# Kernel optimization log

Hardware: AMD Instinct MI355X
Metric: run time of the kernel (lower is better)

The kernel has to match this reference:

```python
import jax, jax.numpy as jnp
import numpy as np

SIG_EPS = 0.1
IN_DIM = 256
OUT_DIM = 64


def setup_inputs() -> dict:
    key = jax.random.key(0)
    ks = jax.random.split(key, 6)
    B, S, Q = 32, 512, 512
    return {
        "phi_support": jax.random.normal(ks[0], (B, S, IN_DIM), jnp.float32),
        "y_support": jax.random.normal(ks[1], (B, S, OUT_DIM), jnp.float32),
        "phi_query": jax.random.normal(ks[2], (B, Q, IN_DIM), jnp.float32),
        "y_query": jax.random.normal(ks[3], (B, Q, OUT_DIM), jnp.float32),
        # learned parameters (K init'd to zeros in torch, use small randn for a non-trivial test)
        "K": jax.random.normal(ks[4], (IN_DIM, OUT_DIM), jnp.float32) * 0.02,
        "L_asym": jax.random.normal(ks[5], (IN_DIM, IN_DIM), jnp.float32) * 0.1,
    }


def reference(phi_support, y_support, phi_query, y_query, K, L_asym):
    sig_eps = jnp.float32(SIG_EPS)
    log_sig_eps = jnp.log(sig_eps)
    out_dim = K.shape[1]

    L = L_asym @ L_asym.T  # [I, I]
    # nobs > 0 branch (n_support = 512)
    posterior_L = jnp.einsum('bsi,bsj->bij', phi_support, phi_support) + L[None]  # [B,I,I]
    posterior_L_inv = jnp.linalg.inv(posterior_L)
    rhs = jnp.einsum('bsi,bso->bio', phi_support, y_support) + (L @ K)[None]  # [B,I,O]
    posterior_K = posterior_L_inv @ rhs  # [B,I,O]

    mu_pred = phi_query @ posterior_K  # [B,Q,O]
    # spread_fac = 1 + diag quadratic form phi Linv phi^T  -> [B,Q]
    spread_fac = 1.0 + jnp.einsum('bqi,bij,bqj->bq', phi_query, posterior_L_inv, phi_query)
    eye_eps = jnp.eye(out_dim, dtype=phi_query.dtype) * sig_eps
    sig_pred = spread_fac[..., None, None] * eye_eps  # [B,Q,O,O]

    # predictive_nll: inverse of sig_pred is an exactly scaled identity, so the
    # quadratic form y^T inv(sig_pred) y == ||y||^2 / (spread_fac * sig_eps) (same math)
    diff = y_query - mu_pred
    quadf = jnp.sum(diff * diff, axis=-1) / (spread_fac * sig_eps)  # [B,Q]
    logdet = out_dim * (jnp.log(spread_fac) + log_sig_eps)  # [B,Q]
    predictive_nll = logdet.mean() + quadf.mean()

    return (mu_pred, sig_pred, predictive_nll)
```

## Files before the change

### kernel.cpp

```cpp
#include <hip/hip_runtime.h>
#include <math.h>

#define B 32
#define S 512
#define Q 512
#define I 256
#define O 64
#define SIG_EPS 0.1f
#define LOG_SIG_EPS (-2.3025850929940457f)

#define WS_L 0
#define WS_T1 65536
#define WS_LKT 81920
#define WS_M0 98304
#define WS_M1 2195456
#define WS_RHST 4292608
#define WS_D 4816896
#define WS_SPF 5079040
#define WS_U16 5095488
#define U_PTH 0
#define U_PTL 4194304
#define U_YTH 8388608
#define U_YTL 9437184
#define U_IVH 10485760
#define U_IVL 12582912

#define OUT_MU_ELEMS (B * Q * O)
#define OUT_SIG_ELEMS (B * Q * O * O)
#define OUT_NLL_IDX (OUT_MU_ELEMS + OUT_SIG_ELEMS)

typedef short short8 __attribute__((ext_vector_type(8)));
typedef float f32x4 __attribute__((ext_vector_type(4)));
#define MFMA16(a, b, c) __builtin_amdgcn_mfma_f32_16x16x32_bf16(a, b, c, 0, 0, 0)

struct Params {
  const float *phi_s, *y_s, *phi_q, *y_q, *Km, *La;
  float *Lm, *T1, *LKT, *M0, *M1, *RHST, *Dbuf, *spws;
  unsigned short *PTh, *PTl, *YTh, *YTl, *IVh, *IVl;
  float *mu, *nll;
  float4 *sig;
};

__device__ __forceinline__ f32x4 mfma3(short8 ah, short8 al, short8 bh, short8 bl, f32x4 c) {
  c = MFMA16(ah, bh, c);
  c = MFMA16(ah, bl, c);
  c = MFMA16(al, bh, c);
  return c;
}

__device__ __forceinline__ unsigned short f2bf(float x) {
  unsigned int u = __float_as_uint(x);
  return (unsigned short)((u + 0x7fffu + ((u >> 16) & 1u)) >> 16);
}
__device__ __forceinline__ float bf2f(unsigned short h) { return __uint_as_float(((unsigned int)h) << 16); }
__device__ __forceinline__ void split2(float x, unsigned short& h, unsigned short& l) {
  h = f2bf(x);
  l = f2bf(x - bf2f(h));
}
__device__ __forceinline__ void split4(float4 v, uint2& H, uint2& L) {
  unsigned short h0, h1, h2, h3, l0, l1, l2, l3;
  split2(v.x, h0, l0); split2(v.y, h1, l1); split2(v.z, h2, l2); split2(v.w, h3, l3);
  H.x = (unsigned)h0 | ((unsigned)h1 << 16); H.y = (unsigned)h2 | ((unsigned)h3 << 16);
  L.x = (unsigned)l0 | ((unsigned)l1 << 16); L.y = (unsigned)l2 | ((unsigned)l3 << 16);
}
__device__ __forceinline__ void cvt8(const float* p, short8& h8, short8& l8) {
  float4 a = *(const float4*)p;
  float4 b = *(const float4*)(p + 4);
  uint2 H0, L0, H1, L1;
  split4(a, H0, L0); split4(b, H1, L1);
  union { uint2 q[2]; short8 s; } uh, ul;
  uh.q[0] = H0; uh.q[1] = H1; ul.q[0] = L0; ul.q[1] = L1;
  h8 = uh.s; l8 = ul.s;
}
__device__ __forceinline__ short8 ld8(const unsigned short* p) { return *(const short8*)(const void*)p; }

__device__ __forceinline__ void fma4x4(const float4 av, const float4 bv, float acc[4][4]) {
  const float ar[4] = {av.x, av.y, av.z, av.w};
  const float br[4] = {bv.x, bv.y, bv.z, bv.w};
#pragma unroll
  for (int i = 0; i < 4; ++i)
#pragma unroll
    for (int j = 0; j < 4; ++j) acc[i][j] += ar[i] * br[j];
}

__device__ __forceinline__ void load_direct64(float* dst, int ds, const float* src, int ss, int t) {
#pragma unroll
  for (int m = 0; m < 4; ++m) {
    int r = (t >> 4) + 16 * m, c4 = (t & 15) * 4;
    *(float4*)&dst[r * ds + c4] = *(const float4*)&src[(size_t)r * ss + c4];
  }
}
__device__ __forceinline__ void load_trans64(float* dst, int ds, const float* src, int ss, int t) {
#pragma unroll
  for (int m = 0; m < 4; ++m) {
    int r = (t >> 4) + 16 * m, c4 = (t & 15) * 4;
    float4 v = *(const float4*)&src[(size_t)r * ss + c4];
    dst[(c4 + 0) * ds + r] = v.x;
    dst[(c4 + 1) * ds + r] = v.y;
    dst[(c4 + 2) * ds + r] = v.z;
    dst[(c4 + 3) * ds + r] = v.w;
  }
}
template <int SA, int SB>
__device__ __forceinline__ void gemm64(const float* At, const float* Bs, int tr, int tc, float acc[4][4]) {
#pragma unroll 8
  for (int kk = 0; kk < 64; ++kk) {
    float4 a = *(const float4*)&At[kk * SA + tr * 4];
    float4 b = *(const float4*)&Bs[kk * SB + tc * 4];
    fma4x4(a, b, acc);
  }
}

#define SC4(V) V.x *= pivinv; V.y *= pivinv; V.z *= pivinv; V.w *= pivinv
#define UP4(V, R) V.x -= g * R.x; V.y -= g * R.y; V.z -= g * R.z; V.w -= g * R.w

template <int TS>
__device__ void gj64(const float* T, float* rowbuf, float* Dout, int t) {
  int r = t >> 2, q = t & 3;
  int lane = t & 63;
  float4 A0 = *(const float4*)&T[r * TS + q * 16 + 0];
  float4 A1 = *(const float4*)&T[r * TS + q * 16 + 4];
  float4 A2 = *(const float4*)&T[r * TS + q * 16 + 8];
  float4 A3 = *(const float4*)&T[r * TS + q * 16 + 12];
#define IC(c) (((q * 16 + (c)) == r) ? 1.f : 0.f)
  float4 I0 = make_float4(IC(0), IC(1), IC(2), IC(3));
  float4 I1 = make_float4(IC(4), IC(5), IC(6), IC(7));
  float4 I2 = make_float4(IC(8), IC(9), IC(10), IC(11));
  float4 I3 = make_float4(IC(12), IC(13), IC(14), IC(15));
#undef IC
  for (int p = 0; p < 64; ++p) {
    float* RA = rowbuf + (p & 1) * 128;
    float* RI = RA + 64;
    if (r == p) {
      ((float4*)&RA[q * 16])[0] = A0; ((float4*)&RA[q * 16])[1] = A1;
      ((float4*)&RA[q * 16])[2] = A2; ((float4*)&RA[q * 16])[3] = A3;
      ((float4*)&RI[q * 16])[0] = I0; ((float4*)&RI[q * 16])[1] = I1;
      ((float4*)&RI[q * 16])[2] = I2; ((float4*)&RI[q * 16])[3] = I3;
    }
    __syncthreads();
    float pivinv = 1.0f / RA[p];
    int sidx = p & 15;
    float4 blk = (sidx < 8) ? ((sidx < 4) ? A0 : A1) : ((sidx < 12) ? A2 : A3);
    int sc = sidx & 3;
    float ap = (sc == 0) ? blk.x : (sc == 1) ? blk.y : (sc == 2) ? blk.z : blk.w;
    float f = __shfl(ap, (lane & ~3) | (p >> 4), 64);
    float4 ra0 = ((const float4*)&RA[q * 16])[0], ra1 = ((const float4*)&RA[q * 16])[1];
    float4 ra2 = ((const float4*)&RA[q * 16])[2], ra3 = ((const float4*)&RA[q * 16])[3];
    float4 ri0 = ((const float4*)&RI[q * 16])[0], ri1 = ((const float4*)&RI[q * 16])[1];
    float4 ri2 = ((const float4*)&RI[q * 16])[2], ri3 = ((const float4*)&RI[q * 16])[3];
    if (r == p) {
      SC4(A0); SC4(A1); SC4(A2); SC4(A3);
      SC4(I0); SC4(I1); SC4(I2); SC4(I3);
    } else {
      float g = f * pivinv;
      UP4(A0, ra0); UP4(A1, ra1); UP4(A2, ra2); UP4(A3, ra3);
      UP4(I0, ri0); UP4(I1, ri1); UP4(I2, ri2); UP4(I3, ri3);
    }
  }
  ((float4*)&Dout[r * 64 + q * 16])[0] = I0;
  ((float4*)&Dout[r * 64 + q * 16])[1] = I1;
  ((float4*)&Dout[r * 64 + q * 16])[2] = I2;
  ((float4*)&Dout[r * 64 + q * 16])[3] = I3;
}

__global__ __launch_bounds__(256) void k_front(Params p) {
  __shared__ float smem[4352];
  int w = blockIdx.x, t = threadIdx.x;
  if (w == 0 && t == 0) p.nll[0] = 0.f;
  if (w < 1280) {
    unsigned short* Hs = (unsigned short*)smem;
    unsigned short* Lo = Hs + 64 * 68;
    const float* src;
    unsigned short *dh, *dl;
    int sstride;
    if (w < 1024) {
      int b = w >> 5, r = w & 31, ic = r >> 3, sc = r & 7;
      src = p.phi_s + ((size_t)b * 512 + sc * 64) * 256 + ic * 64;
      sstride = 256;
      size_t d0 = ((size_t)b * 256 + ic * 64) * 512 + sc * 64;
      dh = p.PTh + d0; dl = p.PTl + d0;
    } else {
      int qq = w - 1024, b = qq >> 3, sc = qq & 7;
      src = p.y_s + ((size_t)b * 512 + sc * 64) * 64;
      sstride = 64;
      size_t d0 = ((size_t)b * 64) * 512 + sc * 64;
      dh = p.YTh + d0; dl = p.YTl + d0;
    }
    int c = t & 63, rb = (t >> 6) * 16;
#pragma unroll
    for (int m = 0; m < 16; ++m) {
      int s = rb + m;
      float x = src[(size_t)s * sstride + c];
      unsigned short h, l;
      split2(x, h, l);
      Hs[c * 68 + s] = h;
      Lo[c * 68 + s] = l;
    }
    __syncthreads();
    int il0 = t >> 4, c4 = (t & 15) * 4;
#pragma unroll
    for (int m = 0; m < 4; ++m) {
      int il = il0 + 16 * m;
      uint2 H, L;
      H.x = (unsigned)Hs[il * 68 + c4] | ((unsigned)Hs[il * 68 + c4 + 1] << 16);
      H.y = (unsigned)Hs[il * 68 + c4 + 2] | ((unsigned)Hs[il * 68 + c4 + 3] << 16);
      L.x = (unsigned)Lo[il * 68 + c4] | ((unsigned)Lo[il * 68 + c4 + 1] << 16);
      L.y = (unsigned)Lo[il * 68 + c4 + 2] | ((unsigned)Lo[il * 68 + c4 + 3] << 16);
      *(uint2*)&dh[(size_t)il * 512 + c4] = H;
      *(uint2*)&dl[(size_t)il * 512 + c4] = L;
    }
  } else {
    int blk2 = w - 1280;
    float* sA = smem;
    float* sB = smem + 1088;
    int tr = t >> 4, tc = t & 15;
    float acc[4][4] = {};
    if (blk2 < 16) {
      int i0 = (blk2 >> 2) * 64, j0 = (blk2 & 3) * 64;
      for (int ks = 0; ks < 256; ks += 16) {
        __syncthreads();
#pragma unroll
        for (int m = 0; m < 4; ++m) {
          int r = (t >> 4) + 16 * m, kk = t & 15;
          sA[kk * 68 + r] = p.La[(size_t)(i0 + r) * 256 + ks + kk];
          sB[kk * 68 + r] = p.La[(size_t)(j0 + r) * 256 + ks + kk];
        }
        __syncthreads();
#pragma unroll
        for (int kk = 0; kk < 16; ++kk) {
          float4 a = *(const float4*)&sA[kk * 68 + tr * 4];
          float4 bv = *(const float4*)&sB[kk * 68 + tc * 4];
          fma4x4(a, bv, acc);
        }
      }
#pragma unroll
      for (int mi = 0; mi < 4; ++mi) {
        float4 v = {acc[mi][0], acc[mi][1], acc[mi][2], acc[mi][3]};
        *(float4*)&p.Lm[(size_t)(i0 + tr * 4 + mi) * 256 + j0 + tc * 4] = v;
      }
    } else {
      int i0 = (blk2 - 16) * 64;
      for (int ks = 0; ks < 256; ks += 16) {
        __syncthreads();
#pragma unroll
        for (int m = 0; m < 4; ++m) {
          int kk = (t >> 6) + 4 * m, c = t & 63;
          sA[kk * 68 + c] = p.La[(size_t)(ks + kk) * 256 + i0 + c];
          sB[kk * 68 + c] = p.Km[(size_t)(ks + kk) * 64 + c];
        }
        __syncthreads();
#pragma unroll
        for (int kk = 0; kk < 16; ++kk) {
          float4 a = *(const float4*)&sA[kk * 68 + tr * 4];
          float4 bv = *(const float4*)&sB[kk * 68 + tc * 4];
          fma4x4(a, bv, acc);
        }
      }
#pragma unroll
      for (int mi = 0; mi < 4; ++mi) {
        float4 v = {acc[mi][0], acc[mi][1], acc[mi][2], acc[mi][3]};
        *(float4*)&p.T1[(size_t)(i0 + tr * 4 + mi) * 64 + tc * 4] = v;
      }
    }
  }
}

__global__ __launch_bounds__(256) void k_gram(Params p) {
  __shared__ float smem[5632];
  float* trbuf = smem;
  float* Ws = smem + 4352;
  float* rowb = smem + 5376;
  int b = blockIdx.x, u = blockIdx.y, t = threadIdx.x;
  if (u == 14) {
    if (b >= 4) return;
    int i0 = b * 64;
    int tr = t >> 4, tc = t & 15;
    float acc[4][4] = {};
    for (int ks = 0; ks < 256; ks += 16) {
      __syncthreads();
#pragma unroll
      for (int m = 0; m < 4; ++m) {
        trbuf[(t & 15) * 68 + (t >> 4) + 16 * m] = p.La[(size_t)(i0 + (t >> 4) + 16 * m) * 256 + ks + (t & 15)];
        Ws[((t >> 6) + 4 * m) * 64 + (t & 63)] = p.T1[(size_t)(ks + (t >> 6) + 4 * m) * 64 + (t & 63)];
      }
      __syncthreads();
#pragma unroll
      for (int kk = 0; kk < 16; ++kk) {
        float4 a = *(const float4*)&trbuf[kk * 68 + tr * 4];
        float4 bv = *(const float4*)&Ws[kk * 64 + tc * 4];
        fma4x4(a, bv, acc);
      }
    }
    __syncthreads();
#pragma unroll
    for (int mi = 0; mi < 4; ++mi)
#pragma unroll
      for (int cj = 0; cj < 4; ++cj) trbuf[(tr * 4 + mi) * 68 + tc * 4 + cj] = acc[mi][cj];
    __syncthreads();
    int rr0 = t >> 4, cc4 = (t & 15) * 4;
#pragma unroll
    for (int m = 0; m < 4; ++m) {
      int rr = rr0 + 16 * m;
      float4 v = {trbuf[(cc4 + 0) * 68 + rr], trbuf[(cc4 + 1) * 68 + rr], trbuf[(cc4 + 2) * 68 + rr],
                  trbuf[(cc4 + 3) * 68 + rr]};
      *(float4*)&p.LKT[(size_t)rr * 256 + i0 + cc4] = v;
    }
    return;
  }
  const int TIa[14] = {0, 0, 0, 0, 1, 1, 1, 2, 2, 3, 0, 1, 2, 3};
  const int TJa[14] = {0, 1, 2, 3, 1, 2, 3, 2, 3, 3, 0, 0, 0, 0};
  bool isR = (u >= 10);
  int it = TIa[u], jt = TJa[u];
  int i0 = it * 64, j0 = isR ? 0 : jt * 64;
  int lane = t & 63, w = t >> 6, wr = w >> 1, wc = w & 1;
  const unsigned short* Ah = p.PTh + (size_t)b * 256 * 512;
  const unsigned short* Al = p.PTl + (size_t)b * 256 * 512;
  const unsigned short* Bh = isR ? (p.YTh + (size_t)b * 64 * 512) : Ah;
  const unsigned short* Bl = isR ? (p.YTl + (size_t)b * 64 * 512) : Al;
  int ra0 = i0 + wr * 32 + (lane & 15);
  int rb0 = j0 + wc * 32 + (lane & 15);
  int klane = (lane >> 4) * 8;
  f32x4 acc[2][2] = {};
  for (int ks = 0; ks < 512; ks += 32) {
    int kk = ks + klane;
    short8 a0h = ld8(Ah + (size_t)ra0 * 512 + kk);
    short8 a1h = ld8(Ah + (size_t)(ra0 + 16) * 512 + kk);
    short8 a0l = ld8(Al + (size_t)ra0 * 512 + kk);
    short8 a1l = ld8(Al + (size_t)(ra0 + 16) * 512 + kk);
    short8 b0h = ld8(Bh + (size_t)rb0 * 512 + kk);
    short8 b1h = ld8(Bh + (size_t)(rb0 + 16) * 512 + kk);
    short8 b0l = ld8(Bl + (size_t)rb0 * 512 + kk);
    short8 b1l = ld8(Bl + (size_t)(rb0 + 16) * 512 + kk);
    acc[0][0] = mfma3(a0h, a0l, b0h, b0l, acc[0][0]);
    acc[0][1] = mfma3(a0h, a0l, b1h, b1l, acc[0][1]);
    acc[1][0] = mfma3(a1h, a1l, b0h, b0l, acc[1][0]);
    acc[1][1] = mfma3(a1h, a1l, b1h, b1l, acc[1][1]);
  }
#pragma unroll
  for (int ti = 0; ti < 2; ++ti)
#pragma unroll
    for (int tj = 0; tj < 2; ++tj)
#pragma unroll
      for (int r = 0; r < 4; ++r)
        trbuf[(wr * 32 + ti * 16 + (lane >> 4) * 4 + r) * 68 + wc * 32 + tj * 16 + (lane & 15)] = acc[ti][tj][r];
  __syncthreads();
  int rr0 = t >> 4, cc4 = (t & 15) * 4;
  if (!isR) {
    float* Mb = p.M0 + (size_t)b * 65536;
    bool d00 = (it == 0 && jt == 0);
#pragma unroll
    for (int m = 0; m < 4; ++m) {
      int rr = rr0 + 16 * m;
      float4 v = *(float4*)&trbuf[rr * 68 + cc4];
      float4 lv = *(const float4*)&p.Lm[(size_t)(i0 + rr) * 256 + j0 + cc4];
      v.x += lv.x; v.y += lv.y; v.z += lv.z; v.w += lv.w;
      *(float4*)&Mb[(size_t)(i0 + rr) * 256 + j0 + cc4] = v;
      if (d00) *(float4*)&trbuf[rr * 68 + cc4] = v;
    }
    if (it != jt) {
#pragma unroll
      for (int m = 0; m < 4; ++m) {
        int rr = rr0 + 16 * m;
        float4 v = {trbuf[(cc4 + 0) * 68 + rr], trbuf[(cc4 + 1) * 68 + rr], trbuf[(cc4 + 2) * 68 + rr],
                    trbuf[(cc4 + 3) * 68 + rr]};
        float4 lv = *(const float4*)&p.Lm[(size_t)(j0 + rr) * 256 + i0 + cc4];
        v.x += lv.x; v.y += lv.y; v.z += lv.z; v.w += lv.w;
        *(float4*)&Mb[(size_t)(j0 + rr) * 256 + i0 + cc4] = v;
      }
    }
    if (d00) {
      __syncthreads();
      gj64<68>(trbuf, rowb, p.Dbuf + (size_t)b * 4096, t);
    }
  } else {
#pragma unroll
    for (int m = 0; m < 4; ++m) {
      int rr = rr0 + 16 * m;
      float4 v = {trbuf[(cc4 + 0) * 68 + rr], trbuf[(cc4 + 1) * 68 + rr], trbuf[(cc4 + 2) * 68 + rr],
                  trbuf[(cc4 + 3) * 68 + rr]};
      *(float4*)&p.RHST[((size_t)b * 64 + rr) * 256 + i0 + cc4] = v;
    }
  }
}

__global__ __launch_bounds__(256) void k_st(Params p, int kb) {
  __shared__ float smem[13056];
  float* shA = smem;
  float* shB = smem + 4352;
  float* shD = smem + 8448;
  float* rowb = smem + 12800;
  int b = blockIdx.x, u = blockIdx.y, t = threadIdx.x;
  if (u == 16) {
    float4* R4 = (float4*)(p.RHST + (size_t)b * 16384);
    const float4* L4 = (const float4*)p.LKT;
#pragma unroll
    for (int m = 0; m < 16; ++m) {
      int idx = m * 256 + t;
      float4 a = R4[idx];
      float4 l = L4[idx];
      a.x += l.x; a.y += l.y; a.z += l.z; a.w += l.w;
      R4[idx] = a;
    }
    return;
  }
  int i = u >> 2, j = u & 3;
  int tr = t >> 4, tc = t & 15;
  const float* Ms = ((kb & 1) ? p.M1 : p.M0) + (size_t)b * 65536;
  float* Md = ((kb & 1) ? p.M0 : p.M1) + (size_t)b * 65536;
  const float* Din = p.Dbuf + (size_t)(kb & 1) * (B * 4096) + (size_t)b * 4096;
  float* Dout = p.Dbuf + (size_t)((kb + 1) & 1) * (B * 4096) + (size_t)b * 4096;
  bool last = (kb == 3);
  unsigned short* Yh = p.IVh + (size_t)b * 65536;
  unsigned short* Yl = p.IVl + (size_t)b * 65536;
  auto STORE = [&](int row, int col, float4 v) {
    if (last) {
      uint2 H, L;
      split4(v, H, L);
      *(uint2*)&Yh[(size_t)row * 256 + col] = H;
      *(uint2*)&Yl[(size_t)row * 256 + col] = L;
    } else {
      *(float4*)&Md[(size_t)row * 256 + col] = v;
    }
  };
  bool ik = (i == kb), jk = (j == kb);
  if (ik && jk) {
#pragma unroll
    for (int m = 0; m < 4; ++m) {
      int r = (t >> 4) + 16 * m, c4 = (t & 15) * 4;
      STORE(kb * 64 + r, kb * 64 + c4, *(const float4*)&Din[r * 64 + c4]);
    }
  } else if (ik) {
    float acc[4][4] = {};
    load_trans64(shA, 68, Din, 64, t);
    load_direct64(shB, 64, &Ms[(size_t)(kb * 64) * 256 + j * 64], 256, t);
    __syncthreads();
    gemm64<68, 64>(shA, shB, tr, tc, acc);
    __syncthreads();
#pragma unroll
    for (int mi = 0; mi < 4; ++mi) {
      float4 v = {acc[mi][0], acc[mi][1], acc[mi][2], acc[mi][3]};
      STORE(kb * 64 + tr * 4 + mi, j * 64 + tc * 4, v);
    }
  } else if (jk) {
    float acc[4][4] = {};
    load_trans64(shA, 68, &Ms[(size_t)(i * 64) * 256 + kb * 64], 256, t);
    load_direct64(shB, 64, Din, 64, t);
    __syncthreads();
    gemm64<68, 64>(shA, shB, tr, tc, acc);
    __syncthreads();
#pragma unroll
    for (int mi = 0; mi < 4; ++mi) {
      float4 v = {-acc[mi][0], -acc[mi][1], -acc[mi][2], -acc[mi][3]};
      STORE(i * 64 + tr * 4 + mi, kb * 64 + tc * 4, v);
    }
  } else {
    float acc[4][4] = {};
    load_trans64(shA, 68, Din, 64, t);
    load_direct64(shB, 64, &Ms[(size_t)(kb * 64) * 256 + j * 64], 256, t);
    load_trans64(shD, 68, &Ms[(size_t)(i * 64) * 256 + kb * 64], 256, t);
    __syncthreads();
    gemm64<68, 64>(shA, shB, tr, tc, acc);
    __syncthreads();
#pragma unroll
    for (int mi = 0; mi < 4; ++mi) {
      float4 v = {acc[mi][0], acc[mi][1], acc[mi][2], acc[mi][3]};
      *(float4*)&shB[(tr * 4 + mi) * 64 + tc * 4] = v;
    }
    __syncthreads();
    float acc2[4][4] = {};
    gemm64<68, 64>(shD, shB, tr, tc, acc2);
    bool la = (kb < 3) && (i == kb + 1) && (j == kb + 1);
    if (la) __syncthreads();
#pragma unroll
    for (int mi = 0; mi < 4; ++mi) {
      size_t off = (size_t)(i * 64 + tr * 4 + mi) * 256 + j * 64 + tc * 4;
      float4 old = *(const float4*)&Ms[off];
      float4 v = {old.x - acc2[mi][0], old.y - acc2[mi][1], old.z - acc2[mi][2], old.w - acc2[mi][3]};
      STORE(i * 64 + tr * 4 + mi, j * 64 + tc * 4, v);
      if (la) *(float4*)&shB[(tr * 4 + mi) * 64 + tc * 4] = v;
    }
    if (la) {
      __syncthreads();
      gj64<64>(shB, rowb, Dout, t);
    }
  }
}

__global__ __launch_bounds__(256) void k_tail(Params p) {
  __shared__ float Xlds[32 * 260];
  __shared__ float Gs[64 * 68];
  __shared__ float spf[32];
  __shared__ float ssdl[32];
  int b = blockIdx.x, qb = blockIdx.y * 32, t = threadIdx.x;
  int lane = t & 63, w = t >> 6;
  int klane = (lane >> 4) * 8;
  const float* Pq = p.phi_q + (size_t)b * 512 * 256;

  short8 ah[2][8], al[2][8];
#pragma unroll
  for (int st = 0; st < 2; ++st) {
    int qlane = qb + st * 16 + (lane & 15);
#pragma unroll
    for (int k8 = 0; k8 < 8; ++k8) cvt8(&Pq[(size_t)qlane * 256 + k8 * 32 + klane], ah[st][k8], al[st][k8]);
  }

  const unsigned short* Vh = p.IVh + (size_t)b * 65536;
  const unsigned short* Vl = p.IVl + (size_t)b * 65536;
  for (int jt = w * 4; jt < w * 4 + 4; ++jt) {
    int jrow = jt * 16 + (lane & 15);
    f32x4 acc0 = {}, acc1 = {};
#pragma unroll
    for (int k8 = 0; k8 < 8; ++k8) {
      short8 bh = ld8(Vh + (size_t)jrow * 256 + k8 * 32 + klane);
      short8 bl = ld8(Vl + (size_t)jrow * 256 + k8 * 32 + klane);
      acc0 = mfma3(ah[0][k8], al[0][k8], bh, bl, acc0);
      acc1 = mfma3(ah[1][k8], al[1][k8], bh, bl, acc1);
    }
    int xi = jt * 16 + (lane & 15);
#pragma unroll
    for (int r = 0; r < 4; ++r) {
      Xlds[((lane >> 4) * 4 + r) * 260 + xi] = acc0[r];
      Xlds[(16 + (lane >> 4) * 4 + r) * 260 + xi] = acc1[r];
    }
  }
  __syncthreads();

  {
    int q = t >> 3, c = t & 7;
    const float* Pqr = Pq + (size_t)(qb + q) * 256;
    float sp = 0.f;
#pragma unroll
    for (int i = c * 32; i < c * 32 + 32; i += 4) {
      float4 xv = *(const float4*)&Xlds[q * 260 + i];
      float4 pv = *(const float4*)&Pqr[i];
      sp += xv.x * pv.x + xv.y * pv.y + xv.z * pv.z + xv.w * pv.w;
    }
    sp += __shfl_xor(sp, 1);
    sp += __shfl_xor(sp, 2);
    sp += __shfl_xor(sp, 4);
    if (c == 0) spf[q] = 1.f + sp;
  }

  {
    int q = t >> 3, c = t & 7;
    const float* Gr = p.RHST + (size_t)b * 16384;
    float accv[8] = {};
    for (int ip = 0; ip < 4; ++ip) {
      __syncthreads();
      int grr = t >> 2, gc = (t & 3) * 16;
#pragma unroll
      for (int m = 0; m < 4; ++m)
        *(float4*)&Gs[grr * 68 + gc + m * 4] = *(const float4*)&Gr[(size_t)grr * 256 + ip * 64 + gc + m * 4];
      __syncthreads();
#pragma unroll 2
      for (int i = 0; i < 64; i += 4) {
        float4 xv = *(const float4*)&Xlds[q * 260 + ip * 64 + i];
#pragma unroll
        for (int oo = 0; oo < 8; ++oo) {
          float4 gv = *(const float4*)&Gs[(c + oo * 8) * 68 + i];
          accv[oo] += xv.x * gv.x + xv.y * gv.y + xv.z * gv.z + xv.w * gv.w;
        }
      }
    }
    size_t qg = (size_t)b * 512 + qb + q;
    float ssd8 = 0.f;
#pragma unroll
    for (int oo = 0; oo < 8; ++oo) {
      int o = c + oo * 8;
      p.mu[qg * 64 + o] = accv[oo];
      float d = p.y_q[qg * 64 + o] - accv[oo];
      ssd8 += d * d;
    }
    ssd8 += __shfl_xor(ssd8, 1);
    ssd8 += __shfl_xor(ssd8, 2);
    ssd8 += __shfl_xor(ssd8, 4);
    if (c == 0) ssdl[q] = ssd8;
  }
  __syncthreads();

  if (w == 0) {
    float val = 0.f;
    if (t < 32) {
      float sp = spf[t];
      val = (64.f * (logf(sp) + LOG_SIG_EPS) + ssdl[t] / (sp * SIG_EPS)) * (1.0f / 16384.0f);
    }
#pragma unroll
    for (int off = 32; off; off >>= 1) val += __shfl_down(val, off);
    if (t == 0) atomicAdd(p.nll, val);
  }
  if (t < 32) p.spws[(size_t)b * 512 + qb + t] = spf[t];
}

__global__ __launch_bounds__(256) void k_sig(const float* __restrict__ spws, float4* __restrict__ sig) {
  size_t idx = (size_t)blockIdx.x * 256 + threadIdx.x;
  int p4 = (int)(idx & 15);
  int o = (int)((idx >> 4) & 63);
  size_t bq = idx >> 10;
  float sv = spws[bq] * SIG_EPS;
  float4 v;
  v.x = (p4 * 4 + 0 == o) ? sv : 0.f;
  v.y = (p4 * 4 + 1 == o) ? sv : 0.f;
  v.z = (p4 * 4 + 2 == o) ? sv : 0.f;
  v.w = (p4 * 4 + 3 == o) ? sv : 0.f;
  sig[idx] = v;
}

extern "C" void kernel_launch(void* const* d_in, const int* in_sizes, int n_in, void* d_out, int out_size,
                              void* d_ws, size_t ws_size, hipStream_t stream) {
  float* ws = (float*)d_ws;
  unsigned short* u16b = (unsigned short*)(ws + WS_U16);
  float* out_mu = (float*)d_out;

  Params p;
  p.phi_s = (const float*)d_in[0];
  p.y_s = (const float*)d_in[1];
  p.phi_q = (const float*)d_in[2];
  p.y_q = (const float*)d_in[3];
  p.Km = (const float*)d_in[4];
  p.La = (const float*)d_in[5];
  p.Lm = ws + WS_L;
  p.T1 = ws + WS_T1;
  p.LKT = ws + WS_LKT;
  p.M0 = ws + WS_M0;
  p.M1 = ws + WS_M1;
  p.RHST = ws + WS_RHST;
  p.Dbuf = ws + WS_D;
  p.spws = ws + WS_SPF;
  p.PTh = u16b + U_PTH;
  p.PTl = u16b + U_PTL;
  p.YTh = u16b + U_YTH;
  p.YTl = u16b + U_YTL;
  p.IVh = u16b + U_IVH;
  p.IVl = u16b + U_IVL;
  p.mu = out_mu;
  p.sig = (float4*)(out_mu + OUT_MU_ELEMS);
  p.nll = out_mu + OUT_NLL_IDX;

  k_front<<<1300, 256, 0, stream>>>(p);
  k_gram<<<dim3(B, 15), 256, 0, stream>>>(p);
  k_st<<<dim3(B, 17), 256, 0, stream>>>(p, 0);
  k_st<<<dim3(B, 16), 256, 0, stream>>>(p, 1);
  k_st<<<dim3(B, 16), 256, 0, stream>>>(p, 2);
  k_st<<<dim3(B, 16), 256, 0, stream>>>(p, 3);
  k_tail<<<dim3(B, 16), 256, 0, stream>>>(p);
  k_sig<<<65536, 256, 0, stream>>>(p.spws, p.sig);
}
```

Baseline: 309.4 us.

## Fuse block Gauss-Jordan pivot steps pairwise and write sig output inside tail kernel

The four per-pivot-block Gauss-Jordan sweeps over the 4x4 block matrix become two launches. Each launch eliminates two pivot blocks at once, redundantly recomputing the second pivot's Schur complement and its 64x64 inverse in every block. Separately, the dense sig_pred diagonal fill moves from its own kernel into k_tail, which removes the spread-factor round trip through workspace. Fewer launches and fewer full passes over the 256x256 matrices are traded for extra per-block GEMMs and a replicated 64x64 inversion in each workgroup, and k_tail now has to write the 268 MB sig output itself.

```diff
diff --git a/kernel.cpp b/kernel.cpp
--- a/kernel.cpp
+++ b/kernel.cpp
@@ -16,7 +16,6 @@
 #define WS_M1 2195456
 #define WS_RHST 4292608
 #define WS_D 4816896
-#define WS_SPF 5079040
 #define WS_U16 5095488
 #define U_PTH 0
 #define U_PTL 4194304
@@ -35,7 +34,7 @@
 
 struct Params {
   const float *phi_s, *y_s, *phi_q, *y_q, *Km, *La;
-  float *Lm, *T1, *LKT, *M0, *M1, *RHST, *Dbuf, *spws;
+  float *Lm, *T1, *LKT, *M0, *M1, *RHST, *Dbuf;
   unsigned short *PTh, *PTl, *YTh, *YTl, *IVh, *IVl;
   float *mu, *nll;
   float4 *sig;
@@ -111,11 +110,52 @@
   }
 }
 
+__device__ __forceinline__ void wr_rm(float* dst, const float a[4][4], int tr, int tc) {
+#pragma unroll
+  for (int mi = 0; mi < 4; ++mi) {
+    float4 v = {a[mi][0], a[mi][1], a[mi][2], a[mi][3]};
+    *(float4*)&dst[(tr * 4 + mi) * 68 + tc * 4] = v;
+  }
+}
+__device__ __forceinline__ void wr_tr(float* dst, const float a[4][4], int tr, int tc) {
+#pragma unroll
+  for (int mi = 0; mi < 4; ++mi)
+#pragma unroll
+    for (int cj = 0; cj < 4; ++cj) dst[(tc * 4 + cj) * 68 + tr * 4 + mi] = a[mi][cj];
+}
+__device__ __forceinline__ void sub_from_g(const float* src, int ss, float a[4][4], int tr, int tc) {
+#pragma unroll
+  for (int mi = 0; mi < 4; ++mi) {
+    float4 g = *(const float4*)&src[(size_t)(tr * 4 + mi) * ss + tc * 4];
+    a[mi][0] = g.x - a[mi][0]; a[mi][1] = g.y - a[mi][1];
+    a[mi][2] = g.z - a[mi][2]; a[mi][3] = g.w - a[mi][3];
+  }
+}
+__device__ __forceinline__ void ld_g(const float* src, int ss, float a[4][4], int tr, int tc) {
+#pragma unroll
+  for (int mi = 0; mi < 4; ++mi) {
+    float4 g = *(const float4*)&src[(size_t)(tr * 4 + mi) * ss + tc * 4];
+    a[mi][0] = g.x; a[mi][1] = g.y; a[mi][2] = g.z; a[mi][3] = g.w;
+  }
+}
+__device__ __forceinline__ void negt(float a[4][4]) {
+#pragma unroll
+  for (int mi = 0; mi < 4; ++mi)
+#pragma unroll
+    for (int cj = 0; cj < 4; ++cj) a[mi][cj] = -a[mi][cj];
+}
+__device__ __forceinline__ void cpt(float d[4][4], const float s[4][4]) {
+#pragma unroll
+  for (int mi = 0; mi < 4; ++mi)
+#pragma unroll
+    for (int cj = 0; cj < 4; ++cj) d[mi][cj] = s[mi][cj];
+}
+
 #define SC4(V) V.x *= pivinv; V.y *= pivinv; V.z *= pivinv; V.w *= pivinv
 #define UP4(V, R) V.x -= g * R.x; V.y -= g * R.y; V.z -= g * R.z; V.w -= g * R.w
 
-template <int TS>
-__device__ void gj64(const float* T, float* rowbuf, float* Dout, int t) {
+template <int TS, int OUT>
+__device__ void gj64c(const float* T, float* rowbuf, float* Dout, int t) {
   int r = t >> 2, q = t & 3;
   int lane = t & 63;
   float4 A0 = *(const float4*)&T[r * TS + q * 16 + 0];
@@ -157,11 +197,20 @@
       UP4(I0, ri0); UP4(I1, ri1); UP4(I2, ri2); UP4(I3, ri3);
     }
   }
-  ((float4*)&Dout[r * 64 + q * 16])[0] = I0;
-  ((float4*)&Dout[r * 64 + q * 16])[1] = I1;
-  ((float4*)&Dout[r * 64 + q * 16])[2] = I2;
-  ((float4*)&Dout[r * 64 + q * 16])[3] = I3;
-}
+  if (OUT == 0) {
+    ((float4*)&Dout[r * 64 + q * 16])[0] = I0;
+    ((float4*)&Dout[r * 64 + q * 16])[1] = I1;
+    ((float4*)&Dout[r * 64 + q * 16])[2] = I2;
+    ((float4*)&Dout[r * 64 + q * 16])[3] = I3;
+  } else {
+    ((float4*)&Dout[r * 68 + q * 16])[0] = I0;
+    ((float4*)&Dout[r * 68 + q * 16])[1] = I1;
+    ((float4*)&Dout[r * 68 + q * 16])[2] = I2;
+    ((float4*)&Dout[r * 68 + q * 16])[3] = I3;
+  }
+}
+template <int TS>
+__device__ void gj64(const float* T, float* rowbuf, float* Dout, int t) { gj64c<TS, 0>(T, rowbuf, Dout, t); }
 
 __global__ __launch_bounds__(256) void k_front(Params p) {
   __shared__ float smem[4352];
@@ -383,12 +432,11 @@
   }
 }
 
-__global__ __launch_bounds__(256) void k_st(Params p, int kb) {
-  __shared__ float smem[13056];
-  float* shA = smem;
-  float* shB = smem + 4352;
-  float* shD = smem + 8448;
-  float* rowb = smem + 12800;
+__global__ __launch_bounds__(256) void k_st2(Params p, int a) {
+  __shared__ float shA[64 * 68];
+  __shared__ float shB[64 * 68];
+  __shared__ float shD[64 * 68];
+  __shared__ float rowb[256];
   int b = blockIdx.x, u = blockIdx.y, t = threadIdx.x;
   if (u == 16) {
     float4* R4 = (float4*)(p.RHST + (size_t)b * 16384);
@@ -396,20 +444,21 @@
 #pragma unroll
     for (int m = 0; m < 16; ++m) {
       int idx = m * 256 + t;
-      float4 a = R4[idx];
-      float4 l = L4[idx];
-      a.x += l.x; a.y += l.y; a.z += l.z; a.w += l.w;
-      R4[idx] = a;
+      float4 av = R4[idx];
+      float4 lv = L4[idx];
+      av.x += lv.x; av.y += lv.y; av.z += lv.z; av.w += lv.w;
+      R4[idx] = av;
     }
     return;
   }
+  int tr = t >> 4, tc = t & 15;
   int i = u >> 2, j = u & 3;
-  int tr = t >> 4, tc = t & 15;
-  const float* Ms = ((kb & 1) ? p.M1 : p.M0) + (size_t)b * 65536;
-  float* Md = ((kb & 1) ? p.M0 : p.M1) + (size_t)b * 65536;
-  const float* Din = p.Dbuf + (size_t)(kb & 1) * (B * 4096) + (size_t)b * 4096;
-  float* Dout = p.Dbuf + (size_t)((kb + 1) & 1) * (B * 4096) + (size_t)b * 4096;
-  bool last = (kb == 3);
+  int b2 = a + 1;
+  const float* Ms = (a == 0 ? p.M0 : p.M1) + (size_t)b * 65536;
+  float* Md = p.M1 + (size_t)b * 65536;
+  const float* Din = p.Dbuf + (a == 0 ? 0 : (size_t)B * 4096) + (size_t)b * 4096;
+  float* DoutG = p.Dbuf + (size_t)B * 4096 + (size_t)b * 4096;
+  bool last = (a == 2);
   unsigned short* Yh = p.IVh + (size_t)b * 65536;
   unsigned short* Yl = p.IVl + (size_t)b * 65536;
   auto STORE = [&](int row, int col, float4 v) {
@@ -422,68 +471,126 @@
       *(float4*)&Md[(size_t)row * 256 + col] = v;
     }
   };
-  bool ik = (i == kb), jk = (j == kb);
-  if (ik && jk) {
-#pragma unroll
-    for (int m = 0; m < 4; ++m) {
-      int r = (t >> 4) + 16 * m, c4 = (t & 15) * 4;
-      STORE(kb * 64 + r, kb * 64 + c4, *(const float4*)&Din[r * 64 + c4]);
-    }
-  } else if (ik) {
-    float acc[4][4] = {};
-    load_trans64(shA, 68, Din, 64, t);
-    load_direct64(shB, 64, &Ms[(size_t)(kb * 64) * 256 + j * 64], 256, t);
-    __syncthreads();
-    gemm64<68, 64>(shA, shB, tr, tc, acc);
-    __syncthreads();
+  auto SACC = [&](const float acc[4][4], int r0, int c0) {
 #pragma unroll
     for (int mi = 0; mi < 4; ++mi) {
       float4 v = {acc[mi][0], acc[mi][1], acc[mi][2], acc[mi][3]};
-      STORE(kb * 64 + tr * 4 + mi, j * 64 + tc * 4, v);
-    }
-  } else if (jk) {
-    float acc[4][4] = {};
-    load_trans64(shA, 68, &Ms[(size_t)(i * 64) * 256 + kb * 64], 256, t);
-    load_direct64(shB, 64, Din, 64, t);
-    __syncthreads();
-    gemm64<68, 64>(shA, shB, tr, tc, acc);
-    __syncthreads();
+      STORE(r0 + tr * 4 + mi, c0 + tc * 4, v);
+    }
+  };
+#define TP(r, c) (&Ms[(size_t)((r) * 64) * 256 + (c) * 64])
+
+  bool isDiag = (i == b2 && j == b2);
+  bool isRow = (i == b2 && j != b2);
+  bool isCol = (j == b2 && i != b2);
+  bool gen = (i != b2 && j != b2);
+  bool needTj = (j != b2 && j != a);
+  bool needDrm = (j == a);
+
+  load_trans64(shA, 68, Din, 64, t);
+  load_direct64(shB, 68, TP(a, b2), 256, t);
+  __syncthreads();
+  float t1c[4][4] = {};
+  gemm64<68, 68>(shA, shB, tr, tc, t1c);
+  float tj[4][4] = {};
+  if (needTj) {
+    __syncthreads();
+    load_direct64(shB, 68, TP(a, j), 256, t);
+    __syncthreads();
+    gemm64<68, 68>(shA, shB, tr, tc, tj);
+    __syncthreads();
+    wr_rm(shB, tj, tr, tc);
+  } else if (needDrm) {
+    __syncthreads();
+    load_direct64(shB, 68, Din, 64, t);
+  }
+  __syncthreads();
+  load_trans64(shD, 68, TP(b2, a), 256, t);
+  wr_rm(shA, t1c, tr, tc);
+  __syncthreads();
+  float sbb[4][4] = {};
+  gemm64<68, 68>(shD, shA, tr, tc, sbb);
+  sub_from_g(TP(b2, b2), 256, sbb, tr, tc);
+  float nbj[4][4] = {};
+  if (gen || isRow) {
+    gemm64<68, 68>(shD, shB, tr, tc, nbj);
+    if (j == a) negt(nbj);
+    else sub_from_g(TP(b2, j), 256, nbj, tr, tc);
+  }
+  float nib[4][4] = {}, nij[4][4] = {};
+  if (gen || isCol) {
+    if (i == a) {
+      cpt(nib, t1c);
+      if (gen) {
+        if (j == a) ld_g(Din, 64, nij, tr, tc);
+        else cpt(nij, tj);
+      }
+    } else {
+      __syncthreads();
+      load_trans64(shD, 68, TP(i, a), 256, t);
+      __syncthreads();
+      gemm64<68, 68>(shD, shA, tr, tc, nib);
+      sub_from_g(TP(i, b2), 256, nib, tr, tc);
+      if (gen) {
+        gemm64<68, 68>(shD, shB, tr, tc, nij);
+        if (j == a) negt(nij);
+        else sub_from_g(TP(i, j), 256, nij, tr, tc);
+      }
+    }
+  }
+  __syncthreads();
+  wr_rm(shA, sbb, tr, tc);
+  __syncthreads();
+  gj64c<68, 1>(shA, rowb, shD, t);
+  __syncthreads();
+  if (isDiag) {
 #pragma unroll
     for (int mi = 0; mi < 4; ++mi) {
-      float4 v = {-acc[mi][0], -acc[mi][1], -acc[mi][2], -acc[mi][3]};
-      STORE(i * 64 + tr * 4 + mi, kb * 64 + tc * 4, v);
-    }
-  } else {
-    float acc[4][4] = {};
-    load_trans64(shA, 68, Din, 64, t);
-    load_direct64(shB, 64, &Ms[(size_t)(kb * 64) * 256 + j * 64], 256, t);
-    load_trans64(shD, 68, &Ms[(size_t)(i * 64) * 256 + kb * 64], 256, t);
-    __syncthreads();
-    gemm64<68, 64>(shA, shB, tr, tc, acc);
-    __syncthreads();
-#pragma unroll
-    for (int mi = 0; mi < 4; ++mi) {
-      float4 v = {acc[mi][0], acc[mi][1], acc[mi][2], acc[mi][3]};
-      *(float4*)&shB[(tr * 4 + mi) * 64 + tc * 4] = v;
-    }
-    __syncthreads();
-    float acc2[4][4] = {};
-    gemm64<68, 64>(shD, shB, tr, tc, acc2);
-    bool la = (kb < 3) && (i == kb + 1) && (j == kb + 1);
-    if (la) __syncthreads();
-#pragma unroll
-    for (int mi = 0; mi < 4; ++mi) {
-      size_t off = (size_t)(i * 64 + tr * 4 + mi) * 256 + j * 64 + tc * 4;
-      float4 old = *(const float4*)&Ms[off];
-      float4 v = {old.x - acc2[mi][0], old.y - acc2[mi][1], old.z - acc2[mi][2], old.w - acc2[mi][3]};
-      STORE(i * 64 + tr * 4 + mi, j * 64 + tc * 4, v);
-      if (la) *(float4*)&shB[(tr * 4 + mi) * 64 + tc * 4] = v;
-    }
-    if (la) {
-      __syncthreads();
-      gj64<64>(shB, rowb, Dout, t);
-    }
-  }
+      float4 v = *(const float4*)&shD[(tr * 4 + mi) * 68 + tc * 4];
+      STORE(b2 * 64 + tr * 4 + mi, b2 * 64 + tc * 4, v);
+    }
+    return;
+  }
+  if (isRow) {
+    wr_rm(shB, nbj, tr, tc);
+    __syncthreads();
+    float pa[4][4] = {};
+    gemm64<68, 68>(shD, shB, tr, tc, pa);
+    SACC(pa, b2 * 64, j * 64);
+    return;
+  }
+  if (isCol) {
+    wr_tr(shB, nib, tr, tc);
+    __syncthreads();
+    float pa[4][4] = {};
+    gemm64<68, 68>(shB, shD, tr, tc, pa);
+    negt(pa);
+    SACC(pa, i * 64, b2 * 64);
+    return;
+  }
+  wr_rm(shB, nbj, tr, tc);
+  __syncthreads();
+  float tp[4][4] = {};
+  gemm64<68, 68>(shD, shB, tr, tc, tp);
+  __syncthreads();
+  wr_tr(shA, nib, tr, tc);
+  wr_rm(shB, tp, tr, tc);
+  __syncthreads();
+  float q4[4][4] = {};
+  gemm64<68, 68>(shA, shB, tr, tc, q4);
+  float pv[4][4];
+#pragma unroll
+  for (int mi = 0; mi < 4; ++mi)
+#pragma unroll
+    for (int cj = 0; cj < 4; ++cj) pv[mi][cj] = nij[mi][cj] - q4[mi][cj];
+  SACC(pv, i * 64, j * 64);
+  if (a == 0 && i == 2 && j == 2) {
+    __syncthreads();
+    wr_rm(shB, pv, tr, tc);
+    __syncthreads();
+    gj64<68>(shB, rowb, DoutG, t);
+  }
+#undef TP
 }
 
 __global__ __launch_bounds__(256) void k_tail(Params p) {
@@ -588,21 +695,22 @@
     for (int off = 32; off; off >>= 1) val += __shfl_down(val, off);
     if (t == 0) atomicAdd(p.nll, val);
   }
-  if (t < 32) p.spws[(size_t)b * 512 + qb + t] = spf[t];
-}
-
-__global__ __launch_bounds__(256) void k_sig(const float* __restrict__ spws, float4* __restrict__ sig) {
-  size_t idx = (size_t)blockIdx.x * 256 + threadIdx.x;
-  int p4 = (int)(idx & 15);
-  int o = (int)((idx >> 4) & 63);
-  size_t bq = idx >> 10;
-  float sv = spws[bq] * SIG_EPS;
-  float4 v;
-  v.x = (p4 * 4 + 0 == o) ? sv : 0.f;
-  v.y = (p4 * 4 + 1 == o) ? sv : 0.f;
-  v.z = (p4 * 4 + 2 == o) ? sv : 0.f;
-  v.w = (p4 * 4 + 3 == o) ? sv : 0.f;
-  sig[idx] = v;
+
+  size_t base = ((size_t)b * 512 + qb) * 1024;
+#pragma unroll 4
+  for (int it = 0; it < 128; ++it) {
+    int idx = it * 256 + t;
+    int rloc = idx >> 10;
+    int o = (idx >> 4) & 63;
+    int p4 = idx & 15;
+    float sv = spf[rloc] * SIG_EPS;
+    float4 v;
+    v.x = (p4 * 4 + 0 == o) ? sv : 0.f;
+    v.y = (p4 * 4 + 1 == o) ? sv : 0.f;
+    v.z = (p4 * 4 + 2 == o) ? sv : 0.f;
+    v.w = (p4 * 4 + 3 == o) ? sv : 0.f;
+    p.sig[base + idx] = v;
+  }
 }
 
 extern "C" void kernel_launch(void* const* d_in, const int* in_sizes, int n_in, void* d_out, int out_size,
@@ -625,7 +733,6 @@
   p.M1 = ws + WS_M1;
   p.RHST = ws + WS_RHST;
   p.Dbuf = ws + WS_D;
-  p.spws = ws + WS_SPF;
   p.PTh = u16b + U_PTH;
   p.PTl = u16b + U_PTL;
   p.YTh = u16b + U_YTH;
@@ -638,10 +745,7 @@
 
   k_front<<<1300, 256, 0, stream>>>(p);
   k_gram<<<dim3(B, 15), 256, 0, stream>>>(p);
-  k_st<<<dim3(B, 17), 256, 0, stream>>>(p, 0);
-  k_st<<<dim3(B, 16), 256, 0, stream>>>(p, 1);
-  k_st<<<dim3(B, 16), 256, 0, stream>>>(p, 2);
-  k_st<<<dim3(B, 16), 256, 0, stream>>>(p, 3);
+  k_st2<<<dim3(B, 17), 256, 0, stream>>>(p, 0);
+  k_st2<<<dim3(B, 16), 256, 0, stream>>>(p, 2);
   k_tail<<<dim3(B, 16), 256, 0, stream>>>(p);
-  k_sig<<<65536, 256, 0, stream>>>(p.spws, p.sig);
-}
+}
```

Result: slower. 331.4 us (+7.1%).

## Fuse bf16 split/transpose of support inputs into gram kernel via LDS staging

Applied to the files above, without the earlier changes.

Removes the separate pre-pass that split phi_support and y_support into hi/lo bf16 transposed copies in global memory. The gram kernel now loads fp32 tiles directly, splits and transposes them into shared memory per 64-row chunk, then runs the MFMA products from LDS. This drops a global write and read of the bf16 copies, but each gram block now redoes the split work for its tiles, since the same phi tile is reprocessed by several blocks. It also adds extra synchronisation and more LDS use per block.

```diff
diff --git a/kernel.cpp b/kernel.cpp
--- a/kernel.cpp
+++ b/kernel.cpp
@@ -18,10 +18,6 @@
 #define WS_D 4816896
 #define WS_SPF 5079040
 #define WS_U16 5095488
-#define U_PTH 0
-#define U_PTL 4194304
-#define U_YTH 8388608
-#define U_YTL 9437184
 #define U_IVH 10485760
 #define U_IVL 12582912
 
@@ -36,7 +32,7 @@
 struct Params {
   const float *phi_s, *y_s, *phi_q, *y_q, *Km, *La;
   float *Lm, *T1, *LKT, *M0, *M1, *RHST, *Dbuf, *spws;
-  unsigned short *PTh, *PTl, *YTh, *YTl, *IVh, *IVl;
+  unsigned short *IVh, *IVl;
   float *mu, *nll;
   float4 *sig;
 };
@@ -163,114 +159,75 @@
   ((float4*)&Dout[r * 64 + q * 16])[3] = I3;
 }
 
-__global__ __launch_bounds__(256) void k_front(Params p) {
-  __shared__ float smem[4352];
-  int w = blockIdx.x, t = threadIdx.x;
-  if (w == 0 && t == 0) p.nll[0] = 0.f;
-  if (w < 1280) {
-    unsigned short* Hs = (unsigned short*)smem;
-    unsigned short* Lo = Hs + 64 * 68;
-    const float* src;
-    unsigned short *dh, *dl;
-    int sstride;
-    if (w < 1024) {
-      int b = w >> 5, r = w & 31, ic = r >> 3, sc = r & 7;
-      src = p.phi_s + ((size_t)b * 512 + sc * 64) * 256 + ic * 64;
-      sstride = 256;
-      size_t d0 = ((size_t)b * 256 + ic * 64) * 512 + sc * 64;
-      dh = p.PTh + d0; dl = p.PTl + d0;
-    } else {
-      int qq = w - 1024, b = qq >> 3, sc = qq & 7;
-      src = p.y_s + ((size_t)b * 512 + sc * 64) * 64;
-      sstride = 64;
-      size_t d0 = ((size_t)b * 64) * 512 + sc * 64;
-      dh = p.YTh + d0; dl = p.YTl + d0;
-    }
-    int c = t & 63, rb = (t >> 6) * 16;
-#pragma unroll
-    for (int m = 0; m < 16; ++m) {
-      int s = rb + m;
-      float x = src[(size_t)s * sstride + c];
-      unsigned short h, l;
-      split2(x, h, l);
-      Hs[c * 68 + s] = h;
-      Lo[c * 68 + s] = l;
-    }
-    __syncthreads();
-    int il0 = t >> 4, c4 = (t & 15) * 4;
-#pragma unroll
-    for (int m = 0; m < 4; ++m) {
-      int il = il0 + 16 * m;
-      uint2 H, L;
-      H.x = (unsigned)Hs[il * 68 + c4] | ((unsigned)Hs[il * 68 + c4 + 1] << 16);
-      H.y = (unsigned)Hs[il * 68 + c4 + 2] | ((unsigned)Hs[il * 68 + c4 + 3] << 16);
-      L.x = (unsigned)Lo[il * 68 + c4] | ((unsigned)Lo[il * 68 + c4 + 1] << 16);
-      L.y = (unsigned)Lo[il * 68 + c4 + 2] | ((unsigned)Lo[il * 68 + c4 + 3] << 16);
-      *(uint2*)&dh[(size_t)il * 512 + c4] = H;
-      *(uint2*)&dl[(size_t)il * 512 + c4] = L;
+__global__ __launch_bounds__(256) void k_pre(Params p) {
+  __shared__ float smem[2176];
+  int blk = blockIdx.x, t = threadIdx.x;
+  if (blk == 0 && t == 0) p.nll[0] = 0.f;
+  float* sA = smem;
+  float* sB = smem + 1088;
+  int tr = t >> 4, tc = t & 15;
+  float acc[4][4] = {};
+  if (blk < 16) {
+    int i0 = (blk >> 2) * 64, j0 = (blk & 3) * 64;
+    for (int ks = 0; ks < 256; ks += 16) {
+      __syncthreads();
+#pragma unroll
+      for (int m = 0; m < 4; ++m) {
+        int r = (t >> 4) + 16 * m, kk = t & 15;
+        sA[kk * 68 + r] = p.La[(size_t)(i0 + r) * 256 + ks + kk];
+        sB[kk * 68 + r] = p.La[(size_t)(j0 + r) * 256 + ks + kk];
+      }
+      __syncthreads();
+#pragma unroll
+      for (int kk = 0; kk < 16; ++kk) {
+        float4 a = *(const float4*)&sA[kk * 68 + tr * 4];
+        float4 bv = *(const float4*)&sB[kk * 68 + tc * 4];
+        fma4x4(a, bv, acc);
+      }
+    }
+#pragma unroll
+    for (int mi = 0; mi < 4; ++mi) {
+      float4 v = {acc[mi][0], acc[mi][1], acc[mi][2], acc[mi][3]};
+      *(float4*)&p.Lm[(size_t)(i0 + tr * 4 + mi) * 256 + j0 + tc * 4] = v;
     }
   } else {
-    int blk2 = w - 1280;
-    float* sA = smem;
-    float* sB = smem + 1088;
-    int tr = t >> 4, tc = t & 15;
-    float acc[4][4] = {};
-    if (blk2 < 16) {
-      int i0 = (blk2 >> 2) * 64, j0 = (blk2 & 3) * 64;
-      for (int ks = 0; ks < 256; ks += 16) {
-        __syncthreads();
-#pragma unroll
-        for (int m = 0; m < 4; ++m) {
-          int r = (t >> 4) + 16 * m, kk = t & 15;
-          sA[kk * 68 + r] = p.La[(size_t)(i0 + r) * 256 + ks + kk];
-          sB[kk * 68 + r] = p.La[(size_t)(j0 + r) * 256 + ks + kk];
-        }
-        __syncthreads();
-#pragma unroll
-        for (int kk = 0; kk < 16; ++kk) {
-          float4 a = *(const float4*)&sA[kk * 68 + tr * 4];
-          float4 bv = *(const float4*)&sB[kk * 68 + tc * 4];
-          fma4x4(a, bv, acc);
-        }
-      }
-#pragma unroll
-      for (int mi = 0; mi < 4; ++mi) {
-        float4 v = {acc[mi][0], acc[mi][1], acc[mi][2], acc[mi][3]};
-        *(float4*)&p.Lm[(size_t)(i0 + tr * 4 + mi) * 256 + j0 + tc * 4] = v;
-      }
-    } else {
-      int i0 = (blk2 - 16) * 64;
-      for (int ks = 0; ks < 256; ks += 16) {
-        __syncthreads();
-#pragma unroll
-        for (int m = 0; m < 4; ++m) {
-          int kk = (t >> 6) + 4 * m, c = t & 63;
-          sA[kk * 68 + c] = p.La[(size_t)(ks + kk) * 256 + i0 + c];
-          sB[kk * 68 + c] = p.Km[(size_t)(ks + kk) * 64 + c];
-        }
-        __syncthreads();
-#pragma unroll
-        for (int kk = 0; kk < 16; ++kk) {
-          float4 a = *(const float4*)&sA[kk * 68 + tr * 4];
-          float4 bv = *(const float4*)&sB[kk * 68 + tc * 4];
-          fma4x4(a, bv, acc);
-        }
-      }
-#pragma unroll
-      for (int mi = 0; mi < 4; ++mi) {
-        float4 v = {acc[mi][0], acc[mi][1], acc[mi][2], acc[mi][3]};
-        *(float4*)&p.T1[(size_t)(i0 + tr * 4 + mi) * 64 + tc * 4] = v;
-      }
+    int i0 = (blk - 16) * 64;
+    for (int ks = 0; ks < 256; ks += 16) {
+      __syncthreads();
+#pragma unroll
+      for (int m = 0; m < 4; ++m) {
+        int kk = (t >> 6) + 4 * m, c = t & 63;
+        sA[kk * 68 + c] = p.La[(size_t)(ks + kk) * 256 + i0 + c];
+        sB[kk * 68 + c] = p.Km[(size_t)(ks + kk) * 64 + c];
+      }
+      __syncthreads();
+#pragma unroll
+      for (int kk = 0; kk < 16; ++kk) {
+        float4 a = *(const float4*)&sA[kk * 68 + tr * 4];
+        float4 bv = *(const float4*)&sB[kk * 68 + tc * 4];
+        fma4x4(a, bv, acc);
+      }
+    }
+#pragma unroll
+    for (int mi = 0; mi < 4; ++mi) {
+      float4 v = {acc[mi][0], acc[mi][1], acc[mi][2], acc[mi][3]};
+      *(float4*)&p.T1[(size_t)(i0 + tr * 4 + mi) * 64 + tc * 4] = v;
     }
   }
 }
 
 __global__ __launch_bounds__(256) void k_gram(Params p) {
-  __shared__ float smem[5632];
-  float* trbuf = smem;
-  float* Ws = smem + 4352;
-  float* rowb = smem + 5376;
+  __shared__ float smemf[5632];
+  __shared__ unsigned short smemu[18432];
+  float* trbuf = smemf;
+  float* rowb = smemf + 4352;
+  float* Ws = smemf + 4608;
+  unsigned short* PAh = smemu;
+  unsigned short* PAl = smemu + 4608;
+  unsigned short* PBh = smemu + 9216;
+  unsigned short* PBl = smemu + 13824;
   int b = blockIdx.x, u = blockIdx.y, t = threadIdx.x;
+
   if (u == 14) {
     if (b >= 4) return;
     int i0 = b * 64;
@@ -307,35 +264,72 @@
     }
     return;
   }
+
   const int TIa[14] = {0, 0, 0, 0, 1, 1, 1, 2, 2, 3, 0, 1, 2, 3};
   const int TJa[14] = {0, 1, 2, 3, 1, 2, 3, 2, 3, 3, 0, 0, 0, 0};
   bool isR = (u >= 10);
   int it = TIa[u], jt = TJa[u];
   int i0 = it * 64, j0 = isR ? 0 : jt * 64;
   int lane = t & 63, w = t >> 6, wr = w >> 1, wc = w & 1;
-  const unsigned short* Ah = p.PTh + (size_t)b * 256 * 512;
-  const unsigned short* Al = p.PTl + (size_t)b * 256 * 512;
-  const unsigned short* Bh = isR ? (p.YTh + (size_t)b * 64 * 512) : Ah;
-  const unsigned short* Bl = isR ? (p.YTl + (size_t)b * 64 * 512) : Al;
-  int ra0 = i0 + wr * 32 + (lane & 15);
-  int rb0 = j0 + wc * 32 + (lane & 15);
+  int ra = wr * 32 + (lane & 15);
+  int rb = wc * 32 + (lane & 15);
   int klane = (lane >> 4) * 8;
+  const float* srcA = p.phi_s + (size_t)b * S * I;
+  const float* srcB;
+  int strB, colB0;
+  if (isR) {
+    srcB = p.y_s + (size_t)b * S * O;
+    strB = O;
+    colB0 = 0;
+  } else {
+    srcB = srcA;
+    strB = I;
+    colB0 = j0;
+  }
+  bool diag = (!isR) && (it == jt);
+  unsigned short* QBh = diag ? PAh : PBh;
+  unsigned short* QBl = diag ? PAl : PBl;
+  int cs = t & 63;
+  int rs0 = (t >> 6) * 16;
+
   f32x4 acc[2][2] = {};
-  for (int ks = 0; ks < 512; ks += 32) {
-    int kk = ks + klane;
-    short8 a0h = ld8(Ah + (size_t)ra0 * 512 + kk);
-    short8 a1h = ld8(Ah + (size_t)(ra0 + 16) * 512 + kk);
-    short8 a0l = ld8(Al + (size_t)ra0 * 512 + kk);
-    short8 a1l = ld8(Al + (size_t)(ra0 + 16) * 512 + kk);
-    short8 b0h = ld8(Bh + (size_t)rb0 * 512 + kk);
-    short8 b1h = ld8(Bh + (size_t)(rb0 + 16) * 512 + kk);
-    short8 b0l = ld8(Bl + (size_t)rb0 * 512 + kk);
-    short8 b1l = ld8(Bl + (size_t)(rb0 + 16) * 512 + kk);
-    acc[0][0] = mfma3(a0h, a0l, b0h, b0l, acc[0][0]);
-    acc[0][1] = mfma3(a0h, a0l, b1h, b1l, acc[0][1]);
-    acc[1][0] = mfma3(a1h, a1l, b0h, b0l, acc[1][0]);
-    acc[1][1] = mfma3(a1h, a1l, b1h, b1l, acc[1][1]);
-  }
+  for (int cc = 0; cc < 8; ++cc) {
+    __syncthreads();
+    int sbase = cc * 64;
+#pragma unroll
+    for (int m = 0; m < 16; ++m) {
+      int s = rs0 + m;
+      float xa = srcA[(size_t)(sbase + s) * I + i0 + cs];
+      unsigned short h, l;
+      split2(xa, h, l);
+      PAh[cs * 72 + s] = h;
+      PAl[cs * 72 + s] = l;
+      if (!diag) {
+        float xb = srcB[(size_t)(sbase + s) * strB + colB0 + cs];
+        split2(xb, h, l);
+        PBh[cs * 72 + s] = h;
+        PBl[cs * 72 + s] = l;
+      }
+    }
+    __syncthreads();
+#pragma unroll
+    for (int ks = 0; ks < 64; ks += 32) {
+      int kk = ks + klane;
+      short8 a0h = ld8(PAh + ra * 72 + kk);
+      short8 a1h = ld8(PAh + (ra + 16) * 72 + kk);
+      short8 a0l = ld8(PAl + ra * 72 + kk);
+      short8 a1l = ld8(PAl + (ra + 16) * 72 + kk);
+      short8 b0h = ld8(QBh + rb * 72 + kk);
+      short8 b1h = ld8(QBh + (rb + 16) * 72 + kk);
+      short8 b0l = ld8(QBl + rb * 72 + kk);
+      short8 b1l = ld8(QBl + (rb + 16) * 72 + kk);
+      acc[0][0] = mfma3(a0h, a0l, b0h, b0l, acc[0][0]);
+      acc[0][1] = mfma3(a0h, a0l, b1h, b1l, acc[0][1]);
+      acc[1][0] = mfma3(a1h, a1l, b0h, b0l, acc[1][0]);
+      acc[1][1] = mfma3(a1h, a1l, b1h, b1l, acc[1][1]);
+    }
+  }
+  __syncthreads();
 #pragma unroll
   for (int ti = 0; ti < 2; ++ti)
 #pragma unroll
@@ -626,17 +620,13 @@
   p.RHST = ws + WS_RHST;
   p.Dbuf = ws + WS_D;
   p.spws = ws + WS_SPF;
-  p.PTh = u16b + U_PTH;
-  p.PTl = u16b + U_PTL;
-  p.YTh = u16b + U_YTH;
-  p.YTl = u16b + U_YTL;
   p.IVh = u16b + U_IVH;
   p.IVl = u16b + U_IVL;
   p.mu = out_mu;
   p.sig = (float4*)(out_mu + OUT_MU_ELEMS);
   p.nll = out_mu + OUT_NLL_IDX;
 
-  k_front<<<1300, 256, 0, stream>>>(p);
+  k_pre<<<20, 256, 0, stream>>>(p);
   k_gram<<<dim3(B, 15), 256, 0, stream>>>(p);
   k_st<<<dim3(B, 17), 256, 0, stream>>>(p, 0);
   k_st<<<dim3(B, 16), 256, 0, stream>>>(p, 1);
```

New measurement: 336.5 us. 8.8% more time.
